# Kernel optimization log

Measured on AMD Instinct MI355X. Metric: run time of the kernel, lower is better.

The kernel has to match this reference:

```python
import jax, jax.numpy as jnp
import numpy as np
from jax import lax

B, C, H, W = 2, 192, 256, 256
HEADS = 6
QC = 4 * C  # elementwise gate: q, gate, k, v
EPS = 1e-12


def setup_inputs() -> dict:
    key = jax.random.key(0)
    ks = jax.random.split(key, 8)
    x = jax.random.normal(ks[0], (B, C, H, W), dtype=jnp.float32)
    qkv_w = jax.random.normal(ks[1], (QC, C), dtype=jnp.float32) * (1.0 / np.sqrt(C))
    qkv_b = jax.random.normal(ks[2], (QC,), dtype=jnp.float32) * 0.02
    dw_w = jax.random.normal(ks[3], (QC, 1, 3, 3), dtype=jnp.float32) * (1.0 / 3.0)
    dw_b = jax.random.normal(ks[4], (QC,), dtype=jnp.float32) * 0.02
    temperature = jnp.ones((HEADS, 1, 1), dtype=jnp.float32)
    proj_w = jax.random.normal(ks[5], (C, C), dtype=jnp.float32) * (1.0 / np.sqrt(C))
    proj_b = jax.random.normal(ks[6], (C,), dtype=jnp.float32) * 0.02
    return {"x": x, "qkv_w": qkv_w, "qkv_b": qkv_b, "dw_w": dw_w, "dw_b": dw_b,
            "temperature": temperature, "proj_w": proj_w, "proj_b": proj_b}


def reference(x, qkv_w, qkv_b, dw_w, dw_b, temperature, proj_w, proj_b):
    b, c, h, w = x.shape
    hd = c // HEADS  # head_dim
    n = h * w
    # 1x1 conv qkv projection
    qkv = jnp.einsum('bchw,oc->bohw', x, qkv_w) + qkv_b[None, :, None, None]
    # 3x3 depthwise conv (groups == channels)
    qkv = lax.conv_general_dilated(
        qkv, dw_w, window_strides=(1, 1), padding=((1, 1), (1, 1)),
        dimension_numbers=('NCHW', 'OIHW', 'NCHW'), feature_group_count=QC)
    qkv = qkv + dw_b[None, :, None, None]
    # split: q, gate (elementwise), k, v
    q = qkv[:, :c]
    gate = qkv[:, c:2 * c]
    k = qkv[:, 2 * c:3 * c]
    v = qkv[:, 3 * c:]
    # b (head c) h w -> b head c (h w)
    def to_heads(t):
        return t.reshape(b, HEADS, hd, n)
    q, k, v, gate = to_heads(q), to_heads(k), to_heads(v), to_heads(gate)
    # L2 normalize along token dim (matches F.normalize eps clamp)
    q = q / jnp.maximum(jnp.sqrt(jnp.sum(q * q, axis=-1, keepdims=True)), EPS)
    k = k / jnp.maximum(jnp.sqrt(jnp.sum(k * k, axis=-1, keepdims=True)), EPS)
    # channel attention: [b, head, hd, hd]
    attn = jnp.einsum('bhcn,bhdn->bhcd', q, k) * temperature[None]
    attn = jax.nn.softmax(attn, axis=-1)
    out = jnp.einsum('bhcd,bhdn->bhcn', attn, v)
    out = out * jax.nn.sigmoid(gate)
    out = out.reshape(b, c, h, w)
    out = jnp.einsum('bchw,oc->bohw', out, proj_w) + proj_b[None, :, None, None]
    return out
```

## Files before the change

kernel.cpp:

```cpp
#include <hip/hip_runtime.h>
#include <math.h>


#define HEADS 6
#define CDIM 192
#define QCH 768
#define HH 256
#define WW 256
#define NPIX 65536
#define PADC 200

typedef __bf16 bf16x8 __attribute__((ext_vector_type(8)));
typedef float f32x4 __attribute__((ext_vector_type(4)));
typedef unsigned short u16x8 __attribute__((ext_vector_type(8)));

__device__ __forceinline__ float b2f(unsigned short u) {
  union { unsigned int i; float f; } x; x.i = ((unsigned int)u) << 16; return x.f;
}
__device__ __forceinline__ unsigned short f2b(float f) {
  union { float f; unsigned int i; } x; x.f = f;
  unsigned int lsb = (x.i >> 16) & 1u;
  x.i += 0x7fffu + lsb;
  return (unsigned short)(x.i >> 16);
}

__global__ void zero_init(float* __restrict__ p, int n) {
  int i = blockIdx.x * 256 + threadIdx.x;
  if (i < n) p[i] = 0.f;
}

__global__ __launch_bounds__(256)
void w2bf(const float* __restrict__ qkv_w, const float* __restrict__ proj_w,
          unsigned short* __restrict__ wbf) {
  int id = blockIdx.x * 256 + threadIdx.x;
  if (id >= 5 * 192 * 192) return;
  int k = id % 192;
  int m = (id / 192) % 192;
  int q = id / (192 * 192);
  float v = (q < 4) ? qkv_w[(size_t)(q * 192 + m) * 192 + k]
                    : proj_w[(size_t)m * 192 + k];
  wbf[((size_t)q * 192 + m) * PADC + k] = f2b(v);
}

__global__ __launch_bounds__(256)
void x2t(const float* __restrict__ x, unsigned short* __restrict__ xT) {
  __shared__ unsigned short tile[64 * PADC];
  int t = threadIdx.x;
  int n0 = blockIdx.x * 64;
  int b = blockIdx.y;
  #pragma unroll
  for (int i = 0; i < 12; ++i) {
    int idx = t + i * 256;
    int c = idx >> 4;
    int nn4 = (idx & 15) << 2;
    float4 v = *(const float4*)(x + ((size_t)b * CDIM + c) * NPIX + n0 + nn4);
    tile[(nn4 + 0) * PADC + c] = f2b(v.x);
    tile[(nn4 + 1) * PADC + c] = f2b(v.y);
    tile[(nn4 + 2) * PADC + c] = f2b(v.z);
    tile[(nn4 + 3) * PADC + c] = f2b(v.w);
  }
  __syncthreads();
  #pragma unroll
  for (int i = 0; i < 6; ++i) {
    int idx = t + i * 256;
    int row = idx / 24;
    int c8 = (idx % 24) * 8;
    *(u16x8*)(xT + ((size_t)b * NPIX + n0 + row) * PADC + c8) =
        *(const u16x8*)(tile + row * PADC + c8);
  }
}

template <int NMT, bool OUT_F32>
__global__ __launch_bounds__(256)
void gemm_t(const unsigned short* __restrict__ wq0,
            const unsigned short* __restrict__ wq1,
            const float* __restrict__ bias0,
            const float* __restrict__ bias1,
            const unsigned short* __restrict__ Bsrc,
            void* __restrict__ outB)
{
  __shared__ unsigned short a_lds[64 * PADC];
  __shared__ unsigned short b_lds[64 * PADC];
  int t = threadIdx.x;
  int n0 = blockIdx.x * 64;
  int b = blockIdx.y;

  const unsigned short* Bs = Bsrc + ((size_t)b * NPIX + n0) * PADC;
  #pragma unroll
  for (int i = 0; i < 6; ++i) {
    int idx = t + i * 256;
    *(u16x8*)(b_lds + idx * 8) = *(const u16x8*)(Bs + (size_t)idx * 8);
  }
  if (t < 64) {
    int idx = 1536 + t;
    *(u16x8*)(b_lds + idx * 8) = *(const u16x8*)(Bs + (size_t)idx * 8);
  }

  int wid = t >> 6, lane = t & 63;
  int r = lane & 15, quad = lane >> 4;

  #pragma unroll
  for (int mt = 0; mt < NMT; ++mt) {
    int half = mt / 3;
    int mrow = (mt % 3) * 64;
    const unsigned short* wq = (half ? wq1 : wq0) + (size_t)mrow * PADC;

    __syncthreads();
    #pragma unroll
    for (int i = 0; i < 6; ++i) {
      int idx = t + i * 256;
      *(u16x8*)(a_lds + idx * 8) = *(const u16x8*)(wq + (size_t)idx * 8);
    }
    if (t < 64) {
      int idx = 1536 + t;
      *(u16x8*)(a_lds + idx * 8) = *(const u16x8*)(wq + (size_t)idx * 8);
    }
    __syncthreads();

    f32x4 acc[4];
    #pragma unroll
    for (int nt = 0; nt < 4; ++nt) acc[nt] = (f32x4){0.f, 0.f, 0.f, 0.f};

    #pragma unroll
    for (int kk = 0; kk < 192; kk += 32) {
      bf16x8 xf = *(const bf16x8*)(b_lds + (wid * 16 + r) * PADC + kk + quad * 8);
      #pragma unroll
      for (int nt = 0; nt < 4; ++nt) {
        bf16x8 wf = *(const bf16x8*)(a_lds + (nt * 16 + r) * PADC + kk + quad * 8);
        acc[nt] = __builtin_amdgcn_mfma_f32_16x16x32_bf16(xf, wf, acc[nt], 0, 0, 0);
      }
    }

    const float* bp = half ? bias1 : bias0;
    size_t n = (size_t)n0 + wid * 16 + quad * 4;
    if (OUT_F32) {
      float* op = (float*)outB + (size_t)b * CDIM * NPIX;
      #pragma unroll
      for (int nt = 0; nt < 4; ++nt) {
        int m = mrow + nt * 16 + r;
        float bb = bp[m];
        float4 vv;
        vv.x = acc[nt][0] + bb; vv.y = acc[nt][1] + bb;
        vv.z = acc[nt][2] + bb; vv.w = acc[nt][3] + bb;
        *(float4*)(op + (size_t)m * NPIX + n) = vv;
      }
    } else {
      unsigned short* op = (unsigned short*)outB +
                           (size_t)(b * 2 + half) * CDIM * NPIX;
      #pragma unroll
      for (int nt = 0; nt < 4; ++nt) {
        int m = mrow + nt * 16 + r;
        float bb = bp[m];
        ushort4 uu;
        uu.x = f2b(acc[nt][0] + bb); uu.y = f2b(acc[nt][1] + bb);
        uu.z = f2b(acc[nt][2] + bb); uu.w = f2b(acc[nt][3] + bb);
        *(ushort4*)(op + (size_t)m * NPIX + n) = uu;
      }
    }
  }
}

__global__ __launch_bounds__(256)
void dwconv_ssq(const unsigned short* __restrict__ in,
                const float* __restrict__ w9,
                const float* __restrict__ bias,
                unsigned short* __restrict__ outp,
                float* __restrict__ ssqBase,
                int qs0, int qs1)
{
  __shared__ unsigned short lds[34][256];
  __shared__ float red[4];
  int t = threadIdx.x;
  int z = blockIdx.z;
  int qsel = (z & 1) ? qs1 : qs0;
  int o  = blockIdx.x >> 3;
  int ry = blockIdx.x & 7;
  int y0 = ry << 5;

  const unsigned short* base = in + ((size_t)z * CDIM + o) * NPIX;
  #pragma unroll
  for (int i = 0; i < 9; ++i) {
    int idx = t + i * 256;
    if (idx < 2176) {
      int row = idx >> 6;
      int c4  = (idx & 63) << 2;
      int gy  = y0 - 1 + row;
      ushort4 vv = make_ushort4(0, 0, 0, 0);
      if (gy >= 0 && gy < HH)
        vv = *(const ushort4*)(base + (size_t)gy * WW + c4);
      *(ushort4*)(&lds[row][c4]) = vv;
    }
  }

  float wv[9];
  #pragma unroll
  for (int i = 0; i < 9; ++i) wv[i] = w9[((size_t)qsel * CDIM + o) * 9 + i];
  float bo = bias[qsel * CDIM + o];
  __syncthreads();

  int w = t >> 6, lane = t & 63;
  int x0 = lane << 2;
  float sumsq = 0.f;
  unsigned short* outbase = outp + ((size_t)z * CDIM + o) * NPIX;

  #pragma unroll
  for (int i = 0; i < 8; ++i) {
    int yo = w * 8 + i;
    float a0 = bo, a1 = bo, a2 = bo, a3 = bo;
    #pragma unroll
    for (int dy = 0; dy < 3; ++dy) {
      ushort4 mv = *(const ushort4*)(&lds[yo + dy][x0]);
      float v0 = b2f(mv.x), v1 = b2f(mv.y), v2 = b2f(mv.z), v3 = b2f(mv.w);
      float vl = __shfl_up(v3, 1, 64);   if (lane == 0)  vl = 0.f;
      float vr = __shfl_down(v0, 1, 64); if (lane == 63) vr = 0.f;
      float w0 = wv[dy * 3 + 0], w1 = wv[dy * 3 + 1], w2 = wv[dy * 3 + 2];
      a0 += w0 * vl + w1 * v0 + w2 * v1;
      a1 += w0 * v0 + w1 * v1 + w2 * v2;
      a2 += w0 * v1 + w1 * v2 + w2 * v3;
      a3 += w0 * v2 + w1 * v3 + w2 * vr;
    }
    ushort4 ov;
    ov.x = f2b(a0); ov.y = f2b(a1); ov.z = f2b(a2); ov.w = f2b(a3);
    *(ushort4*)(outbase + (size_t)(y0 + yo) * WW + x0) = ov;
    if (ssqBase != nullptr) sumsq += a0 * a0 + a1 * a1 + a2 * a2 + a3 * a3;
  }

  if (ssqBase != nullptr) {
    float* ssq = ssqBase + (size_t)(z >> 1) * 2 * CDIM + (z & 1) * CDIM;
    #pragma unroll
    for (int off = 32; off; off >>= 1) sumsq += __shfl_down(sumsq, off, 64);
    if (lane == 0) red[w] = sumsq;
    __syncthreads();
    if (t == 0) atomicAdd(&ssq[o], red[0] + red[1] + red[2] + red[3]);
  }
}

__global__ __launch_bounds__(256)
void gram(const unsigned short* __restrict__ post,
          float* __restrict__ S)
{
  int h = blockIdx.y, b = blockIdx.z;
  int t = threadIdx.x, wid = t >> 6, lane = t & 63;
  int r = lane & 15, quad = lane >> 4;
  int c0 = (wid >> 1) * 16, d0 = (wid & 1) * 16;
  size_t nb = (size_t)blockIdx.x * 512 + quad * 8;
  const unsigned short* qrow =
      post + ((size_t)(b * 2 + 0) * CDIM + h * 32 + c0 + r) * NPIX + nb;
  const unsigned short* krow =
      post + ((size_t)(b * 2 + 1) * CDIM + h * 32 + d0 + r) * NPIX + nb;
  f32x4 acc = (f32x4){0.f, 0.f, 0.f, 0.f};
  #pragma unroll
  for (int kk = 0; kk < 512; kk += 32) {
    bf16x8 af  = *(const bf16x8*)(qrow + kk);
    bf16x8 bfr = *(const bf16x8*)(krow + kk);
    acc = __builtin_amdgcn_mfma_f32_16x16x32_bf16(af, bfr, acc, 0, 0, 0);
  }
  float* Sp = S + ((size_t)b * HEADS + h) * 1024;
  #pragma unroll
  for (int i = 0; i < 4; ++i)
    atomicAdd(&Sp[(c0 + quad * 4 + i) * 32 + (d0 + r)], acc[i]);
}

__global__ void softmax_scale(const float* __restrict__ S,
                              const float* __restrict__ ssq,
                              const float* __restrict__ temp,
                              float* __restrict__ P)
{
  int h = blockIdx.x, b = blockIdx.y;
  int t = threadIdx.x;
  int c = t >> 5, d = t & 31;
  float nq = fmaxf(sqrtf(ssq[(size_t)b * 2 * CDIM + h * 32 + c]), 1e-12f);
  float nk = fmaxf(sqrtf(ssq[(size_t)b * 2 * CDIM + CDIM + h * 32 + d]), 1e-12f);
  float v = S[((size_t)b * HEADS + h) * 1024 + t] / (nq * nk) * temp[h];
  float m = v;
  for (int off = 16; off; off >>= 1) m = fmaxf(m, __shfl_xor(m, off, 32));
  float e = expf(v - m);
  float s = e;
  for (int off = 16; off; off >>= 1) s += __shfl_xor(s, off, 32);
  P[((size_t)b * HEADS + h) * 1024 + t] = e / s;
}

__global__ __launch_bounds__(256)
void pv_gate(const unsigned short* __restrict__ post2,
             const float* __restrict__ P,
             unsigned short* __restrict__ attT)
{
  int h = blockIdx.y, b = blockIdx.z;
  size_t n = (size_t)blockIdx.x * 256 + threadIdx.x;
  const unsigned short* vb = post2 + ((size_t)(b * 2 + 0) * CDIM + h * 32) * NPIX + n;
  const unsigned short* gb = post2 + ((size_t)(b * 2 + 1) * CDIM + h * 32) * NPIX + n;
  const float* Pb = P + ((size_t)b * HEADS + h) * 1024;
  __shared__ float Ps[1024];
  for (int i = threadIdx.x; i < 1024; i += 256) Ps[i] = Pb[i];
  __syncthreads();
  float vr[32];
  #pragma unroll
  for (int d = 0; d < 32; ++d) vr[d] = b2f(vb[(size_t)d * NPIX]);
  unsigned short ub[32];
  #pragma unroll
  for (int c = 0; c < 32; ++c) {
    float a = 0.f;
    #pragma unroll
    for (int d = 0; d < 32; ++d) a += Ps[c * 32 + d] * vr[d];
    float gg = b2f(gb[(size_t)c * NPIX]);
    float sg = 1.f / (1.f + expf(-gg));
    ub[c] = f2b(a * sg);
  }
  unsigned short* op = attT + ((size_t)b * NPIX + n) * PADC + h * 32;
  #pragma unroll
  for (int c8 = 0; c8 < 4; ++c8)
    *(u16x8*)(op + c8 * 8) = *(const u16x8*)(ub + c8 * 8);
}

extern "C" void kernel_launch(void* const* d_in, const int* in_sizes, int n_in,
                              void* d_out, int out_size, void* d_ws, size_t ws_size,
                              hipStream_t stream)
{
  const float* x      = (const float*)d_in[0];
  const float* qkv_w  = (const float*)d_in[1];
  const float* qkv_b  = (const float*)d_in[2];
  const float* dw_w   = (const float*)d_in[3];
  const float* dw_b   = (const float*)d_in[4];
  const float* temp   = (const float*)d_in[5];
  const float* proj_w = (const float*)d_in[6];
  const float* proj_b = (const float*)d_in[7];
  float* out = (float*)d_out;

  char* ws = (char*)d_ws;
  const size_t qbytes  = (size_t)CDIM * NPIX * 2;
  const size_t xTbytes = (size_t)2 * NPIX * PADC * 2;
  const size_t wbytes  = (size_t)5 * 192 * PADC * 2;
  unsigned short* xT    = (unsigned short*)ws;
  unsigned short* wbf   = (unsigned short*)(ws + xTbytes);
  unsigned short* pre   = (unsigned short*)(ws + xTbytes + wbytes);
  unsigned short* post  = (unsigned short*)(ws + xTbytes + wbytes + 4 * qbytes);
  unsigned short* post2 = (unsigned short*)(ws + xTbytes + wbytes + 8 * qbytes);
  unsigned short* attT  = pre;
  float* S   = (float*)(ws + xTbytes + wbytes + 12 * qbytes);
  float* ssq = S + 2 * HEADS * 1024;
  float* P   = ssq + 2 * 2 * CDIM;
  const int nz = 2 * HEADS * 1024 + 2 * 2 * CDIM;

  zero_init<<<(nz + 255) / 256, 256, 0, stream>>>(S, nz);
  w2bf<<<(5 * 192 * 192 + 255) / 256, 256, 0, stream>>>(qkv_w, proj_w, wbf);
  x2t<<<dim3(NPIX / 64, 2), 256, 0, stream>>>(x, xT);

  const unsigned short* wq = wbf;
  const size_t wqs = (size_t)192 * PADC;

  gemm_t<6, false><<<dim3(NPIX / 64, 2), 256, 0, stream>>>(
      wq + 0 * wqs, wq + 2 * wqs, qkv_b + 0 * CDIM, qkv_b + 2 * CDIM, xT, pre);
  dwconv_ssq<<<dim3(CDIM * 8, 1, 4), 256, 0, stream>>>(pre, dw_w, dw_b, post, ssq, 0, 2);

  gemm_t<6, false><<<dim3(NPIX / 64, 2), 256, 0, stream>>>(
      wq + 3 * wqs, wq + 1 * wqs, qkv_b + 3 * CDIM, qkv_b + 1 * CDIM, xT, pre);
  dwconv_ssq<<<dim3(CDIM * 8, 1, 4), 256, 0, stream>>>(pre, dw_w, dw_b, post2, nullptr, 3, 1);

  gram<<<dim3(128, HEADS, 2), 256, 0, stream>>>(post, S);
  softmax_scale<<<dim3(HEADS, 2), 1024, 0, stream>>>(S, ssq, temp, P);

  pv_gate<<<dim3(NPIX / 256, HEADS, 2), 256, 0, stream>>>(post2, P, attT);

  gemm_t<3, true><<<dim3(NPIX / 64, 2), 256, 0, stream>>>(
      wq + 4 * wqs, wq + 4 * wqs, proj_b, proj_b, attT, out);
}
```

Measured before the change: 574.5 us.

## Write attention output per-head contiguous and read P directly in pv_gate

pv_gate now writes its output into a per-head layout [b][head][n][32], so each thread stores 64 contiguous bytes into a compact buffer instead of a 32-channel slice of a padded 200-wide row. The projection GEMM gets a new load mode that gathers the six head slices back into the padded LDS tile. pv_gate also drops its shared-memory staging of P and its barrier, reading P with uniform float4 loads straight from global memory and relying on the cache. This trades LDS traffic and a sync for more global or scalar loads of P inside the inner loop.

```diff
diff --git a/kernel.cpp b/kernel.cpp
--- a/kernel.cpp
+++ b/kernel.cpp
@@ -70,7 +70,7 @@
   }
 }
 
-template <int NMT, bool OUT_F32>
+template <int NMT, bool OUT_F32, int BL>
 __global__ __launch_bounds__(256)
 void gemm_t(const unsigned short* __restrict__ wq0,
             const unsigned short* __restrict__ wq1,
@@ -85,15 +85,27 @@
   int n0 = blockIdx.x * 64;
   int b = blockIdx.y;
 
-  const unsigned short* Bs = Bsrc + ((size_t)b * NPIX + n0) * PADC;
-  #pragma unroll
-  for (int i = 0; i < 6; ++i) {
-    int idx = t + i * 256;
-    *(u16x8*)(b_lds + idx * 8) = *(const u16x8*)(Bs + (size_t)idx * 8);
-  }
-  if (t < 64) {
-    int idx = 1536 + t;
-    *(u16x8*)(b_lds + idx * 8) = *(const u16x8*)(Bs + (size_t)idx * 8);
+  if (BL == 0) {
+    const unsigned short* Bs = Bsrc + ((size_t)b * NPIX + n0) * PADC;
+    #pragma unroll
+    for (int i = 0; i < 6; ++i) {
+      int idx = t + i * 256;
+      *(u16x8*)(b_lds + idx * 8) = *(const u16x8*)(Bs + (size_t)idx * 8);
+    }
+    if (t < 64) {
+      int idx = 1536 + t;
+      *(u16x8*)(b_lds + idx * 8) = *(const u16x8*)(Bs + (size_t)idx * 8);
+    }
+  } else {
+    const unsigned short* Bs = Bsrc + (size_t)b * HEADS * NPIX * 32;
+    #pragma unroll
+    for (int i = 0; i < 6; ++i) {
+      int idx = t + i * 256;
+      int row = idx / 24, cp = idx % 24;
+      int h = cp >> 2, d8 = cp & 3;
+      *(u16x8*)(b_lds + row * PADC + cp * 8) =
+          *(const u16x8*)(Bs + ((size_t)h * NPIX + n0 + row) * 32 + d8 * 8);
+    }
   }
 
   int wid = t >> 6, lane = t & 63;
@@ -289,24 +301,37 @@
   size_t n = (size_t)blockIdx.x * 256 + threadIdx.x;
   const unsigned short* vb = post2 + ((size_t)(b * 2 + 0) * CDIM + h * 32) * NPIX + n;
   const unsigned short* gb = post2 + ((size_t)(b * 2 + 1) * CDIM + h * 32) * NPIX + n;
-  const float* Pb = P + ((size_t)b * HEADS + h) * 1024;
-  __shared__ float Ps[1024];
-  for (int i = threadIdx.x; i < 1024; i += 256) Ps[i] = Pb[i];
-  __syncthreads();
+  const float* Prow = P + ((size_t)b * HEADS + h) * 1024;
+
   float vr[32];
   #pragma unroll
   for (int d = 0; d < 32; ++d) vr[d] = b2f(vb[(size_t)d * NPIX]);
+
   unsigned short ub[32];
   #pragma unroll
   for (int c = 0; c < 32; ++c) {
-    float a = 0.f;
-    #pragma unroll
-    for (int d = 0; d < 32; ++d) a += Ps[c * 32 + d] * vr[d];
+    const float4 p0 = *(const float4*)(Prow + c * 32 + 0);
+    const float4 p1 = *(const float4*)(Prow + c * 32 + 4);
+    const float4 p2 = *(const float4*)(Prow + c * 32 + 8);
+    const float4 p3 = *(const float4*)(Prow + c * 32 + 12);
+    const float4 p4 = *(const float4*)(Prow + c * 32 + 16);
+    const float4 p5 = *(const float4*)(Prow + c * 32 + 20);
+    const float4 p6 = *(const float4*)(Prow + c * 32 + 24);
+    const float4 p7 = *(const float4*)(Prow + c * 32 + 28);
+    float a = p0.x * vr[0]  + p0.y * vr[1]  + p0.z * vr[2]  + p0.w * vr[3]
+            + p1.x * vr[4]  + p1.y * vr[5]  + p1.z * vr[6]  + p1.w * vr[7]
+            + p2.x * vr[8]  + p2.y * vr[9]  + p2.z * vr[10] + p2.w * vr[11]
+            + p3.x * vr[12] + p3.y * vr[13] + p3.z * vr[14] + p3.w * vr[15]
+            + p4.x * vr[16] + p4.y * vr[17] + p4.z * vr[18] + p4.w * vr[19]
+            + p5.x * vr[20] + p5.y * vr[21] + p5.z * vr[22] + p5.w * vr[23]
+            + p6.x * vr[24] + p6.y * vr[25] + p6.z * vr[26] + p6.w * vr[27]
+            + p7.x * vr[28] + p7.y * vr[29] + p7.z * vr[30] + p7.w * vr[31];
     float gg = b2f(gb[(size_t)c * NPIX]);
     float sg = 1.f / (1.f + expf(-gg));
     ub[c] = f2b(a * sg);
   }
-  unsigned short* op = attT + ((size_t)b * NPIX + n) * PADC + h * 32;
+
+  unsigned short* op = attT + (((size_t)(b * HEADS + h) * NPIX) + n) * 32;
   #pragma unroll
   for (int c8 = 0; c8 < 4; ++c8)
     *(u16x8*)(op + c8 * 8) = *(const u16x8*)(ub + c8 * 8);
@@ -348,11 +373,11 @@
   const unsigned short* wq = wbf;
   const size_t wqs = (size_t)192 * PADC;
 
-  gemm_t<6, false><<<dim3(NPIX / 64, 2), 256, 0, stream>>>(
+  gemm_t<6, false, 0><<<dim3(NPIX / 64, 2), 256, 0, stream>>>(
       wq + 0 * wqs, wq + 2 * wqs, qkv_b + 0 * CDIM, qkv_b + 2 * CDIM, xT, pre);
   dwconv_ssq<<<dim3(CDIM * 8, 1, 4), 256, 0, stream>>>(pre, dw_w, dw_b, post, ssq, 0, 2);
 
-  gemm_t<6, false><<<dim3(NPIX / 64, 2), 256, 0, stream>>>(
+  gemm_t<6, false, 0><<<dim3(NPIX / 64, 2), 256, 0, stream>>>(
       wq + 3 * wqs, wq + 1 * wqs, qkv_b + 3 * CDIM, qkv_b + 1 * CDIM, xT, pre);
   dwconv_ssq<<<dim3(CDIM * 8, 1, 4), 256, 0, stream>>>(pre, dw_w, dw_b, post2, nullptr, 3, 1);
 
@@ -361,6 +386,6 @@
 
   pv_gate<<<dim3(NPIX / 256, HEADS, 2), 256, 0, stream>>>(post2, P, attT);
 
-  gemm_t<3, true><<<dim3(NPIX / 64, 2), 256, 0, stream>>>(
+  gemm_t<3, true, 1><<<dim3(NPIX / 64, 2), 256, 0, stream>>>(
       wq + 4 * wqs, wq + 4 * wqs, proj_b, proj_b, attT, out);
 }
```

Result: faster. 531.6 us (-7.5%).

## Fuse attention-V product and sigmoid gate into projection GEMM via MFMA

Applied to the files above, without the earlier changes.

Removes the separate pv_gate kernel and the attT intermediate. The new proj_fused kernel computes P·V with bf16 MFMA per head, applies the sigmoid gate, writes the result straight into LDS, and then runs the output projection GEMM from there. Softmax now writes P in bf16 so it can feed the MFMA directly. This saves a global write and read of the attention output and turns scalar FMA work into matrix instructions. In exchange, V and gate are loaded with strided scalar accesses, and P is rounded to bf16, which lowers precision slightly.

```diff
diff --git a/kernel.cpp b/kernel.cpp
--- a/kernel.cpp
+++ b/kernel.cpp
@@ -70,14 +70,14 @@
   }
 }
 
-template <int NMT, bool OUT_F32>
+template <int NMT>
 __global__ __launch_bounds__(256)
 void gemm_t(const unsigned short* __restrict__ wq0,
             const unsigned short* __restrict__ wq1,
             const float* __restrict__ bias0,
             const float* __restrict__ bias1,
             const unsigned short* __restrict__ Bsrc,
-            void* __restrict__ outB)
+            unsigned short* __restrict__ outB)
 {
   __shared__ unsigned short a_lds[64 * PADC];
   __shared__ unsigned short b_lds[64 * PADC];
@@ -133,29 +133,102 @@
 
     const float* bp = half ? bias1 : bias0;
     size_t n = (size_t)n0 + wid * 16 + quad * 4;
-    if (OUT_F32) {
-      float* op = (float*)outB + (size_t)b * CDIM * NPIX;
+    unsigned short* op = outB + (size_t)(b * 2 + half) * CDIM * NPIX;
+    #pragma unroll
+    for (int nt = 0; nt < 4; ++nt) {
+      int m = mrow + nt * 16 + r;
+      float bb = bp[m];
+      ushort4 uu;
+      uu.x = f2b(acc[nt][0] + bb); uu.y = f2b(acc[nt][1] + bb);
+      uu.z = f2b(acc[nt][2] + bb); uu.w = f2b(acc[nt][3] + bb);
+      *(ushort4*)(op + (size_t)m * NPIX + n) = uu;
+    }
+  }
+}
+
+__global__ __launch_bounds__(256)
+void proj_fused(const unsigned short* __restrict__ wproj,
+                const float* __restrict__ bias,
+                const unsigned short* __restrict__ post2,
+                const unsigned short* __restrict__ Pbf,
+                float* __restrict__ out)
+{
+  __shared__ unsigned short a_lds[64 * PADC];
+  __shared__ unsigned short b_lds[64 * PADC];
+  int t = threadIdx.x;
+  int n0 = blockIdx.x * 64;
+  int b = blockIdx.y;
+  int wid = t >> 6, lane = t & 63;
+  int r = lane & 15, quad = lane >> 4;
+  int nl = wid * 16 + r;
+  size_t n = (size_t)n0 + nl;
+
+  const unsigned short* vbase = post2 + (size_t)(b * 2 + 0) * CDIM * NPIX;
+  const unsigned short* gbase = post2 + (size_t)(b * 2 + 1) * CDIM * NPIX;
+  const unsigned short* Pb = Pbf + (size_t)b * HEADS * 1024;
+
+  #pragma unroll
+  for (int h = 0; h < HEADS; ++h) {
+    union { unsigned short u[8]; bf16x8 v; } vf;
+    #pragma unroll
+    for (int j = 0; j < 8; ++j)
+      vf.u[j] = vbase[(size_t)(h * 32 + quad * 8 + j) * NPIX + n];
+    #pragma unroll
+    for (int c0 = 0; c0 < 32; c0 += 16) {
+      bf16x8 pf = *(const bf16x8*)(Pb + h * 1024 + (c0 + r) * 32 + quad * 8);
+      f32x4 d = (f32x4){0.f, 0.f, 0.f, 0.f};
+      d = __builtin_amdgcn_mfma_f32_16x16x32_bf16(pf, vf.v, d, 0, 0, 0);
+      #pragma unroll
+      for (int i = 0; i < 4; ++i) {
+        int c = c0 + quad * 4 + i;
+        float gg = b2f(gbase[(size_t)(h * 32 + c) * NPIX + n]);
+        float sg = 1.f / (1.f + expf(-gg));
+        b_lds[nl * PADC + h * 32 + c] = f2b(d[i] * sg);
+      }
+    }
+  }
+
+  #pragma unroll
+  for (int mt = 0; mt < 3; ++mt) {
+    int mrow = mt * 64;
+    const unsigned short* wq = wproj + (size_t)mrow * PADC;
+
+    __syncthreads();
+    #pragma unroll
+    for (int i = 0; i < 6; ++i) {
+      int idx = t + i * 256;
+      *(u16x8*)(a_lds + idx * 8) = *(const u16x8*)(wq + (size_t)idx * 8);
+    }
+    if (t < 64) {
+      int idx = 1536 + t;
+      *(u16x8*)(a_lds + idx * 8) = *(const u16x8*)(wq + (size_t)idx * 8);
+    }
+    __syncthreads();
+
+    f32x4 acc[4];
+    #pragma unroll
+    for (int nt = 0; nt < 4; ++nt) acc[nt] = (f32x4){0.f, 0.f, 0.f, 0.f};
+
+    #pragma unroll
+    for (int kk = 0; kk < 192; kk += 32) {
+      bf16x8 xf = *(const bf16x8*)(b_lds + (wid * 16 + r) * PADC + kk + quad * 8);
       #pragma unroll
       for (int nt = 0; nt < 4; ++nt) {
-        int m = mrow + nt * 16 + r;
-        float bb = bp[m];
-        float4 vv;
-        vv.x = acc[nt][0] + bb; vv.y = acc[nt][1] + bb;
-        vv.z = acc[nt][2] + bb; vv.w = acc[nt][3] + bb;
-        *(float4*)(op + (size_t)m * NPIX + n) = vv;
+        bf16x8 wf = *(const bf16x8*)(a_lds + (nt * 16 + r) * PADC + kk + quad * 8);
+        acc[nt] = __builtin_amdgcn_mfma_f32_16x16x32_bf16(xf, wf, acc[nt], 0, 0, 0);
       }
-    } else {
-      unsigned short* op = (unsigned short*)outB +
-                           (size_t)(b * 2 + half) * CDIM * NPIX;
-      #pragma unroll
-      for (int nt = 0; nt < 4; ++nt) {
-        int m = mrow + nt * 16 + r;
-        float bb = bp[m];
-        ushort4 uu;
-        uu.x = f2b(acc[nt][0] + bb); uu.y = f2b(acc[nt][1] + bb);
-        uu.z = f2b(acc[nt][2] + bb); uu.w = f2b(acc[nt][3] + bb);
-        *(ushort4*)(op + (size_t)m * NPIX + n) = uu;
-      }
+    }
+
+    size_t nn = (size_t)n0 + wid * 16 + quad * 4;
+    float* op = out + (size_t)b * CDIM * NPIX;
+    #pragma unroll
+    for (int nt = 0; nt < 4; ++nt) {
+      int m = mrow + nt * 16 + r;
+      float bb = bias[m];
+      float4 vv;
+      vv.x = acc[nt][0] + bb; vv.y = acc[nt][1] + bb;
+      vv.z = acc[nt][2] + bb; vv.w = acc[nt][3] + bb;
+      *(float4*)(op + (size_t)m * NPIX + nn) = vv;
     }
   }
 }
@@ -264,7 +337,7 @@
 __global__ void softmax_scale(const float* __restrict__ S,
                               const float* __restrict__ ssq,
                               const float* __restrict__ temp,
-                              float* __restrict__ P)
+                              unsigned short* __restrict__ Pbf)
 {
   int h = blockIdx.x, b = blockIdx.y;
   int t = threadIdx.x;
@@ -277,39 +350,7 @@
   float e = expf(v - m);
   float s = e;
   for (int off = 16; off; off >>= 1) s += __shfl_xor(s, off, 32);
-  P[((size_t)b * HEADS + h) * 1024 + t] = e / s;
-}
-
-__global__ __launch_bounds__(256)
-void pv_gate(const unsigned short* __restrict__ post2,
-             const float* __restrict__ P,
-             unsigned short* __restrict__ attT)
-{
-  int h = blockIdx.y, b = blockIdx.z;
-  size_t n = (size_t)blockIdx.x * 256 + threadIdx.x;
-  const unsigned short* vb = post2 + ((size_t)(b * 2 + 0) * CDIM + h * 32) * NPIX + n;
-  const unsigned short* gb = post2 + ((size_t)(b * 2 + 1) * CDIM + h * 32) * NPIX + n;
-  const float* Pb = P + ((size_t)b * HEADS + h) * 1024;
-  __shared__ float Ps[1024];
-  for (int i = threadIdx.x; i < 1024; i += 256) Ps[i] = Pb[i];
-  __syncthreads();
-  float vr[32];
-  #pragma unroll
-  for (int d = 0; d < 32; ++d) vr[d] = b2f(vb[(size_t)d * NPIX]);
-  unsigned short ub[32];
-  #pragma unroll
-  for (int c = 0; c < 32; ++c) {
-    float a = 0.f;
-    #pragma unroll
-    for (int d = 0; d < 32; ++d) a += Ps[c * 32 + d] * vr[d];
-    float gg = b2f(gb[(size_t)c * NPIX]);
-    float sg = 1.f / (1.f + expf(-gg));
-    ub[c] = f2b(a * sg);
-  }
-  unsigned short* op = attT + ((size_t)b * NPIX + n) * PADC + h * 32;
-  #pragma unroll
-  for (int c8 = 0; c8 < 4; ++c8)
-    *(u16x8*)(op + c8 * 8) = *(const u16x8*)(ub + c8 * 8);
+  Pbf[((size_t)b * HEADS + h) * 1024 + c * 32 + d] = f2b(e / s);
 }
 
 extern "C" void kernel_launch(void* const* d_in, const int* in_sizes, int n_in,
@@ -335,10 +376,9 @@
   unsigned short* pre   = (unsigned short*)(ws + xTbytes + wbytes);
   unsigned short* post  = (unsigned short*)(ws + xTbytes + wbytes + 4 * qbytes);
   unsigned short* post2 = (unsigned short*)(ws + xTbytes + wbytes + 8 * qbytes);
-  unsigned short* attT  = pre;
   float* S   = (float*)(ws + xTbytes + wbytes + 12 * qbytes);
   float* ssq = S + 2 * HEADS * 1024;
-  float* P   = ssq + 2 * 2 * CDIM;
+  unsigned short* Pbf = (unsigned short*)(ssq + 2 * 2 * CDIM);
   const int nz = 2 * HEADS * 1024 + 2 * 2 * CDIM;
 
   zero_init<<<(nz + 255) / 256, 256, 0, stream>>>(S, nz);
@@ -348,19 +388,17 @@
   const unsigned short* wq = wbf;
   const size_t wqs = (size_t)192 * PADC;
 
-  gemm_t<6, false><<<dim3(NPIX / 64, 2), 256, 0, stream>>>(
+  gemm_t<6><<<dim3(NPIX / 64, 2), 256, 0, stream>>>(
       wq + 0 * wqs, wq + 2 * wqs, qkv_b + 0 * CDIM, qkv_b + 2 * CDIM, xT, pre);
   dwconv_ssq<<<dim3(CDIM * 8, 1, 4), 256, 0, stream>>>(pre, dw_w, dw_b, post, ssq, 0, 2);
 
-  gemm_t<6, false><<<dim3(NPIX / 64, 2), 256, 0, stream>>>(
+  gemm_t<6><<<dim3(NPIX / 64, 2), 256, 0, stream>>>(
       wq + 3 * wqs, wq + 1 * wqs, qkv_b + 3 * CDIM, qkv_b + 1 * CDIM, xT, pre);
   dwconv_ssq<<<dim3(CDIM * 8, 1, 4), 256, 0, stream>>>(pre, dw_w, dw_b, post2, nullptr, 3, 1);
 
   gram<<<dim3(128, HEADS, 2), 256, 0, stream>>>(post, S);
-  softmax_scale<<<dim3(HEADS, 2), 1024, 0, stream>>>(S, ssq, temp, P);
-
-  pv_gate<<<dim3(NPIX / 256, HEADS, 2), 256, 0, stream>>>(post2, P, attT);
-
-  gemm_t<3, true><<<dim3(NPIX / 64, 2), 256, 0, stream>>>(
-      wq + 4 * wqs, wq + 4 * wqs, proj_b, proj_b, attT, out);
-}
+  softmax_scale<<<dim3(HEADS, 2), 1024, 0, stream>>>(S, ssq, temp, Pbf);
+
+  proj_fused<<<dim3(NPIX / 64, 2), 256, 0, stream>>>(
+      wq + 4 * wqs, proj_b, post2, Pbf, out);
+}
```

After: 507.3 us. -11.7%, faster.
